# Kernel optimization log

Measured on AMD Instinct MI355X. Metric: run time of the kernel, lower is better.

## Reference

```python
import jax, jax.numpy as jnp
import numpy as np

D = 1024
H = 16
DH = D // H
F = 4096
B, S = 4, 2048
EPS = 1e-5


def _ln(x, g, b):
    m = jnp.mean(x, axis=-1, keepdims=True)
    v = jnp.var(x, axis=-1, keepdims=True)
    return (x - m) * jax.lax.rsqrt(v + EPS) * g + b


def setup_inputs() -> dict:
    key = jax.random.key(0)
    ks = jax.random.split(key, 16)
    s = 0.02
    return {
        "x": jax.random.normal(ks[0], (B, S, D), jnp.float32),
        "key_padding_mask": jnp.zeros((B, S), jnp.bool_),
        "Wq": jax.random.normal(ks[1], (D, D), jnp.float32) * s,
        "bq": jnp.zeros((D,), jnp.float32),
        "Wk": jax.random.normal(ks[2], (D, D), jnp.float32) * s,
        "bk": jnp.zeros((D,), jnp.float32),
        "Wv": jax.random.normal(ks[3], (D, D), jnp.float32) * s,
        "bv": jnp.zeros((D,), jnp.float32),
        "Wo": jax.random.normal(ks[4], (D, D), jnp.float32) * s,
        "bo": jnp.zeros((D,), jnp.float32),
        "W1": jax.random.normal(ks[5], (F, D), jnp.float32) * s,
        "b1": jnp.zeros((F,), jnp.float32),
        "W2": jax.random.normal(ks[6], (D, F), jnp.float32) * s,
        "b2": jnp.zeros((D,), jnp.float32),
        "ln1_g": jnp.ones((D,), jnp.float32),
        "ln1_b": jnp.zeros((D,), jnp.float32),
        "ln2_g": jnp.ones((D,), jnp.float32),
        "ln2_b": jnp.zeros((D,), jnp.float32),
    }


def _attn(x, kpm, Wq, bq, Wk, bk, Wv, bv, Wo, bo):
    b, s, d = x.shape
    scaling = DH ** (-0.5)
    q = (x @ Wq.T + bq) * scaling
    k = x @ Wk.T + bk
    v = x @ Wv.T + bv
    q = q.reshape(b, s, H, DH)
    k = k.reshape(b, s, H, DH)
    v = v.reshape(b, s, H, DH)
    # [b,h,q,k]
    scores = jnp.einsum("bqhd,bkhd->bhqk", q, k)
    scores = jnp.where(kpm[:, None, None, :], -jnp.inf, scores)
    p = jax.nn.softmax(scores.astype(jnp.float32), axis=-1).astype(q.dtype)
    out = jnp.einsum("bhqk,bkhd->bqhd", p, v).reshape(b, s, d)
    return out @ Wo.T + bo


def reference(x, key_padding_mask, Wq, bq, Wk, bk, Wv, bv, Wo, bo,
              W1, b1, W2, b2, ln1_g, ln1_b, ln2_g, ln2_b):
    # post-LN (normalize_before=False), dropout in eval mode (identity)
    x = _ln(x + _attn(x, key_padding_mask, Wq, bq, Wk, bk, Wv, bv, Wo, bo), ln1_g, ln1_b)
    h = jax.nn.gelu(x @ W1.T + b1, approximate=False)
    x = _ln(x + (h @ W2.T + b2), ln2_g, ln2_b)
    return x
```

## Files before the change

kernel.cpp:

```cpp
#include <hip/hip_runtime.h>
#include <hip/hip_bf16.h>
#include <math.h>

typedef short bf16x8 __attribute__((ext_vector_type(8)));
typedef float f32x4 __attribute__((ext_vector_type(4)));
typedef float f32x2 __attribute__((ext_vector_type(2)));

__device__ __forceinline__ unsigned short f2bfu(float f) {
    __hip_bfloat16 h = __float2bfloat16(f);
    return __builtin_bit_cast(unsigned short, h);
}

__device__ __forceinline__ float fexp2(float x) {
    float r;
    asm("v_exp_f32 %0, %1" : "=v"(r) : "v"(x));
    return r;
}

__device__ __forceinline__ unsigned cvtpk_bf16(float lo, float hi) {
    unsigned r;
    asm("v_cvt_pk_bf16_f32 %0, %1, %2" : "=v"(r) : "v"(lo), "v"(hi));
    return r;
}

__device__ __forceinline__ float max3f(float a, float b, float c) {
    float r;
    asm("v_max3_f32 %0, %1, %2, %3" : "=v"(r) : "v"(a), "v"(b), "v"(c));
    return r;
}

__device__ __forceinline__ f32x2 pk_sub2(f32x2 a, f32x2 b) {
    f32x2 r;
    asm("v_pk_add_f32 %0, %1, %2 neg_lo:[0,1] neg_hi:[0,1]" : "=v"(r) : "v"(a), "v"(b));
    return r;
}

__device__ __forceinline__ f32x2 pk_add2(f32x2 a, f32x2 b) {
    f32x2 r;
    asm("v_pk_add_f32 %0, %1, %2" : "=v"(r) : "v"(a), "v"(b));
    return r;
}

__device__ __forceinline__ float gelu_fast(float x) {
    const float x2 = x * x;
    const float z = x * (0.7978845608f + 0.0356774081f * x2);
    const float e = fexp2(z * 2.88539008f);
    const float r = __builtin_amdgcn_rcpf(e + 1.0f);
    return x * (1.0f - r);
}

__device__ __forceinline__ void gload_lds16(const void* gsrc, void* ldst) {
    __builtin_amdgcn_global_load_lds((const __attribute__((address_space(1))) void*)gsrc,
                                     (__attribute__((address_space(3))) void*)ldst,
                                     16, 0, 0);
}

#define MFMA __builtin_amdgcn_mfma_f32_16x16x32_bf16

__global__ __launch_bounds__(256)
void cvt_all_kernel(const float4* __restrict__ x,  ushort4* __restrict__ xb,
                    const float4* __restrict__ wq, ushort4* __restrict__ wqb,
                    const float4* __restrict__ wk, ushort4* __restrict__ wkb,
                    const float4* __restrict__ wv, ushort4* __restrict__ wvb,
                    const float4* __restrict__ wo, ushort4* __restrict__ wob,
                    const float4* __restrict__ w1, ushort4* __restrict__ w1b,
                    const float4* __restrict__ w2, ushort4* __restrict__ w2b)
{
    const int i = blockIdx.x * 256 + threadIdx.x;
    const float4* src;
    ushort4* dst;
    int base;
    if (i < 2097152)      { src = x;  dst = xb;  base = 0; }
    else if (i < 2359296) { src = wq; dst = wqb; base = 2097152; }
    else if (i < 2621440) { src = wk; dst = wkb; base = 2359296; }
    else if (i < 2883584) { src = wv; dst = wvb; base = 2621440; }
    else if (i < 3145728) { src = wo; dst = wob; base = 2883584; }
    else if (i < 4194304) { src = w1; dst = w1b; base = 3145728; }
    else                  { src = w2; dst = w2b; base = 4194304; }
    const float4 v = src[i - base];
    ushort4 o;
    o.x = f2bfu(v.x); o.y = f2bfu(v.y); o.z = f2bfu(v.z); o.w = f2bfu(v.w);
    dst[i - base] = o;
}

enum { EPI_QKV = 0, EPI_RES_OB = 2, EPI_GELU = 3 };

template<int EPI>
__global__ __launch_bounds__(256, 3)
void gemm_bt(const __hip_bfloat16* __restrict__ A,
             const __hip_bfloat16* __restrict__ W,
             const float* __restrict__ bias,
             const void* __restrict__ resv,
             float scale,
             void* __restrict__ outp, void* __restrict__ outp2, void* __restrict__ outp3,
             int M, int N, int K)
{
    __shared__ __hip_bfloat16 As[3][128 * 32];
    __shared__ __hip_bfloat16 Ws[3][128 * 32];
    const int tid = threadIdx.x;
    const int lane = tid & 63;
    const int wid = tid >> 6;
    const int wr = wid >> 1, wc = wid & 1;
    const int g = lane >> 4, lr = lane & 15;
    const int row0 = blockIdx.x * 128;
    const int col0 = blockIdx.y * 128;

    f32x4 acc[4][4];
    const f32x4 zero = {0.f, 0.f, 0.f, 0.f};
#pragma unroll
    for (int m = 0; m < 4; ++m)
#pragma unroll
        for (int n = 0; n < 4; ++n) acc[m][n] = zero;

    const int c0 = tid, c1 = tid + 256;
    const int ar0 = c0 >> 2, ac0 = (c0 & 3) * 8;
    const int ar1 = c1 >> 2, ac1 = (c1 & 3) * 8;
    const __hip_bfloat16* Arow0 = A + (size_t)(row0 + ar0) * K + ac0;
    const __hip_bfloat16* Arow1 = A + (size_t)(row0 + ar1) * K + ac1;
    const __hip_bfloat16* Wrow0 = W + (size_t)(col0 + ar0) * K + ac0;
    const __hip_bfloat16* Wrow1 = W + (size_t)(col0 + ar1) * K + ac1;

    auto stage = [&](int bi, int k0) {
        gload_lds16(Arow0 + k0, (char*)As[bi] + c0 * 16);
        gload_lds16(Arow1 + k0, (char*)As[bi] + c1 * 16);
        gload_lds16(Wrow0 + k0, (char*)Ws[bi] + c0 * 16);
        gload_lds16(Wrow1 + k0, (char*)Ws[bi] + c1 * 16);
    };

    const int NT = K >> 5;
    stage(0, 0);
    stage(1, 32);
    asm volatile("s_waitcnt vmcnt(4)" ::: "memory");
    __builtin_amdgcn_s_barrier();
    __builtin_amdgcn_sched_barrier(0);

    int cur = 0, stg = 2;
    int kpre = 64;
    for (int t = 0; t < NT; ++t) {
        if (t + 2 < NT) stage(stg, kpre);

        bf16x8 af[4], wf[4];
#pragma unroll
        for (int m = 0; m < 4; ++m)
            af[m] = *(const bf16x8*)(As[cur] + (wr * 64 + m * 16 + lr) * 32 + g * 8);
#pragma unroll
        for (int n = 0; n < 4; ++n)
            wf[n] = *(const bf16x8*)(Ws[cur] + (wc * 64 + n * 16 + lr) * 32 + g * 8);
#pragma unroll
        for (int m = 0; m < 4; ++m)
#pragma unroll
            for (int n = 0; n < 4; ++n)
                acc[m][n] = MFMA(af[m], wf[n], acc[m][n], 0, 0, 0);

        if (t + 1 < NT) {
            if (t + 2 < NT) asm volatile("s_waitcnt vmcnt(4)" ::: "memory");
            else            asm volatile("s_waitcnt vmcnt(0)" ::: "memory");
            __builtin_amdgcn_s_barrier();
            __builtin_amdgcn_sched_barrier(0);
        }
        cur = (cur == 2) ? 0 : cur + 1;
        stg = (stg == 2) ? 0 : stg + 1;
        kpre += 32;
    }

#pragma unroll
    for (int n = 0; n < 4; ++n) {
        const int cc = col0 + wc * 64 + n * 16 + lr;
        const float bv = bias[cc];
#pragma unroll
        for (int m = 0; m < 4; ++m) {
            const int rbase = row0 + wr * 64 + m * 16 + g * 4;
            if (EPI == EPI_QKV) {
                const int seg = col0 >> 10;
                if (seg == 2) {
                    ushort4 u;
                    u.x = f2bfu(acc[m][n][0] + bv);
                    u.y = f2bfu(acc[m][n][1] + bv);
                    u.z = f2bfu(acc[m][n][2] + bv);
                    u.w = f2bfu(acc[m][n][3] + bv);
                    const int cc2 = cc - 2048;
                    const int h_ = cc2 >> 6, dh = cc2 & 63;
                    const int bb = rbase >> 11;
                    const int s = rbase & 2047;
                    *(ushort4*)((__hip_bfloat16*)outp3 +
                                (((size_t)bb * 16 + h_) * 64 + dh) * 2048 + s) = u;
                } else {
                    const float sc = (seg == 0) ? scale : 1.0f;
                    __hip_bfloat16* dst = (seg == 0) ? (__hip_bfloat16*)outp
                                                     : (__hip_bfloat16*)outp2;
                    const int ccl = cc & 1023;
#pragma unroll
                    for (int r = 0; r < 4; ++r)
                        dst[(size_t)(rbase + r) * 1024 + ccl] =
                            __float2bfloat16((acc[m][n][r] + bv) * sc);
                }
            } else {
#pragma unroll
                for (int r = 0; r < 4; ++r) {
                    const size_t idx = (size_t)(rbase + r) * N + cc;
                    float v = acc[m][n][r] + bv;
                    if (EPI == EPI_RES_OB) {
                        const float rv = __bfloat162float(((const __hip_bfloat16*)resv)[idx]);
                        ((__hip_bfloat16*)outp)[idx] = __float2bfloat16(v + rv);
                    } else if (EPI == EPI_GELU) {
                        ((__hip_bfloat16*)outp)[idx] = __float2bfloat16(gelu_fast(v));
                    }
                }
            }
        }
    }
}

__global__ __launch_bounds__(512, 4)
void attn_flash3(const __hip_bfloat16* __restrict__ Q,
                 const __hip_bfloat16* __restrict__ K,
                 const __hip_bfloat16* __restrict__ VT,
                 const unsigned char* __restrict__ kpm,
                 __hip_bfloat16* __restrict__ O)
{
    __shared__ __hip_bfloat16 Ks[2][64 * 64];
    __shared__ __hip_bfloat16 VTs[2][64 * 64];
    __shared__ __hip_bfloat16 Plds[8][32 * 64];

    const int tid = threadIdx.x;
    const int lane = tid & 63;
    const int w = tid >> 6;
    const int g = lane >> 4, lr = lane & 15;

    const int orig = blockIdx.y * 8 + blockIdx.x;
    const int nl = (orig & 7) * 64 + (orig >> 3);
    const int qb = nl & 7;
    const int bh = nl >> 3;

    const int b = bh >> 4, h = bh & 15;
    const int q0 = qb * 256 + w * 32;
    const size_t tokbase = (size_t)b * 2048;
    const __hip_bfloat16* VTbh = VT + (size_t)bh * 64 * 2048;

    unsigned tmask = 0;
#pragma unroll
    for (int i = 0; i < 8; ++i) {
        const unsigned mv = *(const unsigned*)(kpm + tokbase + i * 256 + lane * 4);
        const unsigned long long bal = __ballot((int)(mv != 0u));
#pragma unroll
        for (int j = 0; j < 4; ++j)
            if ((bal >> (16 * j)) & 0xFFFFull) tmask |= (1u << (i * 4 + j));
    }

    bf16x8 qf[2][2];
#pragma unroll
    for (int qn = 0; qn < 2; ++qn)
#pragma unroll
        for (int f = 0; f < 2; ++f)
            qf[qn][f] = *(const bf16x8*)(Q + (tokbase + q0 + qn * 16 + lr) * 1024 +
                                         h * 64 + f * 32 + g * 8);

    f32x4 o[2][4];
    const f32x4 zero = {0.f, 0.f, 0.f, 0.f};
#pragma unroll
    for (int qa = 0; qa < 2; ++qa)
#pragma unroll
        for (int nd = 0; nd < 4; ++nd) o[qa][nd] = zero;
    float m_run[2], l_part[2];
#pragma unroll
    for (int qn = 0; qn < 2; ++qn) { m_run[qn] = -1e30f; l_part[qn] = 0.f; }

    __hip_bfloat16* Pw = Plds[w];

    const int srow = w * 8 + (lane >> 3);
    const int sblk = (lane & 7) ^ (srow & 7);
    const __hip_bfloat16* Ksrc = K + (tokbase + srow) * 1024 + h * 64 + sblk * 8;
    const __hip_bfloat16* Vsrc = VTbh + (size_t)srow * 2048 + sblk * 8;

    auto stage = [&](int bufi, int kv0) {
        gload_lds16(Ksrc + (size_t)kv0 * 1024, (char*)&Ks[bufi][w * 512] + lane * 16);
        gload_lds16(Vsrc + kv0, (char*)&VTs[bufi][w * 512] + lane * 16);
    };

    stage(0, 0);
    __syncthreads();
    int buf = 0;

    for (int t = 0; t < 32; ++t) {
        const int kv0 = t * 64;
        if (t < 31) stage(buf ^ 1, kv0 + 64);

        f32x4 st[4][2];
        __builtin_amdgcn_s_setprio(1);
#pragma unroll
        for (int km = 0; km < 4; ++km) {
            bf16x8 kf[2];
#pragma unroll
            for (int f = 0; f < 2; ++f)
                kf[f] = *(const bf16x8*)(&Ks[buf][(km * 16 + lr) * 64 +
                                                  (((f * 4 + g) ^ (lr & 7)) * 8)]);
#pragma unroll
            for (int qn = 0; qn < 2; ++qn) {
                st[km][qn] = MFMA(kf[0], qf[qn][0], zero, 0, 0, 0);
                st[km][qn] = MFMA(kf[1], qf[qn][1], st[km][qn], 0, 0, 0);
            }
        }
        __builtin_amdgcn_s_setprio(0);

        if (tmask & (1u << t)) {
            const float NEG = -1e30f;
#pragma unroll
            for (int km = 0; km < 4; ++km) {
                const unsigned mu = *(const unsigned*)(kpm + tokbase + kv0 + km * 16 + g * 4);
#pragma unroll
                for (int r = 0; r < 4; ++r) {
                    if ((mu >> (8 * r)) & 0xFFu) {
#pragma unroll
                        for (int qn = 0; qn < 2; ++qn) st[km][qn][r] = NEG;
                    }
                }
            }
        }

        float pm[2];
#pragma unroll
        for (int qn = 0; qn < 2; ++qn) {
            const float v1 = max3f(st[0][qn][0], st[0][qn][1], st[0][qn][2]);
            const float v2 = max3f(st[0][qn][3], st[1][qn][0], st[1][qn][1]);
            const float v3 = max3f(st[1][qn][2], st[1][qn][3], st[2][qn][0]);
            const float v4 = max3f(st[2][qn][1], st[2][qn][2], st[2][qn][3]);
            const float v5 = max3f(st[3][qn][0], st[3][qn][1], st[3][qn][2]);
            pm[qn] = fmaxf(max3f(v1, v2, v3), max3f(v4, v5, st[3][qn][3]));
        }
        const int trig = (pm[0] > m_run[0] + 8.f) | (pm[1] > m_run[1] + 8.f);
        if (__any(trig)) {
            float alpha_q[2];
#pragma unroll
            for (int qn = 0; qn < 2; ++qn) {
                float rm = pm[qn];
                rm = fmaxf(rm, __shfl_xor(rm, 16));
                rm = fmaxf(rm, __shfl_xor(rm, 32));
                const float mnew = fmaxf(m_run[qn], rm);
                const float al = fexp2(m_run[qn] - mnew);
                l_part[qn] *= al;
                m_run[qn] = mnew;
                alpha_q[qn] = al;
            }
#pragma unroll
            for (int qa = 0; qa < 2; ++qa)
#pragma unroll
                for (int r = 0; r < 4; ++r) {
                    const float av = __shfl(alpha_q[qa], g * 4 + r, 16);
#pragma unroll
                    for (int nd = 0; nd < 4; ++nd) o[qa][nd][r] *= av;
                }
        }

#pragma unroll
        for (int qn = 0; qn < 2; ++qn) {
            const float mm = m_run[qn];
            const f32x2 mm2 = {mm, mm};
            f32x2 lacc = {0.f, 0.f};
#pragma unroll
            for (int km = 0; km < 4; ++km) {
                const f32x2 s01 = {st[km][qn][0], st[km][qn][1]};
                const f32x2 s23 = {st[km][qn][2], st[km][qn][3]};
                const f32x2 d01 = pk_sub2(s01, mm2);
                const f32x2 d23 = pk_sub2(s23, mm2);
                f32x2 p01, p23;
                p01.x = fexp2(d01.x);
                p01.y = fexp2(d01.y);
                p23.x = fexp2(d23.x);
                p23.y = fexp2(d23.y);
                lacc = pk_add2(lacc, pk_add2(p01, p23));
                uint2 pk;
                pk.x = cvtpk_bf16(p01.x, p01.y);
                pk.y = cvtpk_bf16(p23.x, p23.y);
                const int cs = (km * 2 + (g >> 1)) ^ (lr & 7);
                *(uint2*)(Pw + (qn * 16 + lr) * 64 + cs * 8 + (g & 1) * 4) = pk;
            }
            l_part[qn] += lacc.x + lacc.y;
        }

        __builtin_amdgcn_s_setprio(1);
#pragma unroll
        for (int f = 0; f < 2; ++f) {
            bf16x8 pa[2];
#pragma unroll
            for (int qa = 0; qa < 2; ++qa)
                pa[qa] = *(const bf16x8*)(Pw + (qa * 16 + lr) * 64 +
                                          (((f * 4 + g) ^ (lr & 7)) * 8));
#pragma unroll
            for (int nd = 0; nd < 4; ++nd) {
                bf16x8 vb = *(const bf16x8*)(&VTs[buf][(nd * 16 + lr) * 64 +
                                                       (((f * 4 + g) ^ (lr & 7)) * 8)]);
#pragma unroll
                for (int qa = 0; qa < 2; ++qa)
                    o[qa][nd] = MFMA(pa[qa], vb, o[qa][nd], 0, 0, 0);
            }
        }
        __builtin_amdgcn_s_setprio(0);

        __syncthreads();
        buf ^= 1;
    }

    float linv[2];
#pragma unroll
    for (int qn = 0; qn < 2; ++qn) {
        float lt = l_part[qn];
        lt += __shfl_xor(lt, 16);
        lt += __shfl_xor(lt, 32);
        linv[qn] = 1.0f / lt;
    }
#pragma unroll
    for (int qa = 0; qa < 2; ++qa)
#pragma unroll
        for (int r = 0; r < 4; ++r) {
            const float lv = __shfl(linv[qa], g * 4 + r, 16);
            const size_t row = tokbase + q0 + qa * 16 + g * 4 + r;
#pragma unroll
            for (int nd = 0; nd < 4; ++nd)
                O[row * 1024 + h * 64 + nd * 16 + lr] = __float2bfloat16(o[qa][nd][r] * lv);
        }
}

__global__ __launch_bounds__(256)
void ln_b_kernel(const __hip_bfloat16* __restrict__ in, const float* __restrict__ gamma,
                 const float* __restrict__ beta, float* __restrict__ outf,
                 __hip_bfloat16* __restrict__ outb)
{
    const int row = blockIdx.x;
    const int tid = threadIdx.x;
    const ushort4 u = ((const ushort4*)(in + (size_t)row * 1024))[tid];
    float v0 = __bfloat162float(__builtin_bit_cast(__hip_bfloat16, u.x));
    float v1 = __bfloat162float(__builtin_bit_cast(__hip_bfloat16, u.y));
    float v2 = __bfloat162float(__builtin_bit_cast(__hip_bfloat16, u.z));
    float v3 = __bfloat162float(__builtin_bit_cast(__hip_bfloat16, u.w));
    float s = (v0 + v1) + (v2 + v3);
    float s2 = (v0 * v0 + v1 * v1) + (v2 * v2 + v3 * v3);
#pragma unroll
    for (int off = 1; off < 64; off <<= 1) {
        s += __shfl_xor(s, off);
        s2 += __shfl_xor(s2, off);
    }
    __shared__ float red[8];
    const int wv = tid >> 6;
    if ((tid & 63) == 0) { red[wv] = s; red[4 + wv] = s2; }
    __syncthreads();
    s = red[0] + red[1] + red[2] + red[3];
    s2 = red[4] + red[5] + red[6] + red[7];
    const float mean = s * (1.f / 1024.f);
    const float var = s2 * (1.f / 1024.f) - mean * mean;
    const float rstd = rsqrtf(var + 1e-5f);
    const float4 gm = ((const float4*)gamma)[tid];
    const float4 bt = ((const float4*)beta)[tid];
    float y0 = (v0 - mean) * rstd * gm.x + bt.x;
    float y1 = (v1 - mean) * rstd * gm.y + bt.y;
    float y2 = (v2 - mean) * rstd * gm.z + bt.z;
    float y3 = (v3 - mean) * rstd * gm.w + bt.w;
    if (outf) {
        float4 y; y.x = y0; y.y = y1; y.z = y2; y.w = y3;
        ((float4*)(outf + (size_t)row * 1024))[tid] = y;
    }
    if (outb) {
        ushort4 ub;
        ub.x = f2bfu(y0); ub.y = f2bfu(y1); ub.z = f2bfu(y2); ub.w = f2bfu(y3);
        ((ushort4*)outb)[row * 256 + tid] = ub;
    }
}

extern "C" void kernel_launch(void* const* d_in, const int* in_sizes, int n_in,
                              void* d_out, int out_size, void* d_ws, size_t ws_size,
                              hipStream_t stream)
{
    const float* x    = (const float*)d_in[0];
    const unsigned char* kpm = (const unsigned char*)d_in[1];
    const float* Wq = (const float*)d_in[2];
    const float* bq = (const float*)d_in[3];
    const float* Wk = (const float*)d_in[4];
    const float* bk = (const float*)d_in[5];
    const float* Wv = (const float*)d_in[6];
    const float* bv = (const float*)d_in[7];
    const float* Wo = (const float*)d_in[8];
    const float* bo = (const float*)d_in[9];
    const float* W1 = (const float*)d_in[10];
    const float* b1 = (const float*)d_in[11];
    const float* W2 = (const float*)d_in[12];
    const float* b2 = (const float*)d_in[13];
    const float* ln1g = (const float*)d_in[14];
    const float* ln1b = (const float*)d_in[15];
    const float* ln2g = (const float*)d_in[16];
    const float* ln2b = (const float*)d_in[17];
    float* out = (float*)d_out;

    char* ws = (char*)d_ws;
    const size_t SZ_ND2 = (size_t)8192 * 1024 * 2;
    size_t off = 0;
    __hip_bfloat16* xb  = (__hip_bfloat16*)(ws + off); off += SZ_ND2;
    __hip_bfloat16* wqb = (__hip_bfloat16*)(ws + off); off += (size_t)1024 * 1024 * 2;
    __hip_bfloat16* wkb = (__hip_bfloat16*)(ws + off); off += (size_t)1024 * 1024 * 2;
    __hip_bfloat16* wvb = (__hip_bfloat16*)(ws + off); off += (size_t)1024 * 1024 * 2;
    __hip_bfloat16* wob = (__hip_bfloat16*)(ws + off); off += (size_t)1024 * 1024 * 2;
    __hip_bfloat16* w1b = (__hip_bfloat16*)(ws + off); off += (size_t)4096 * 1024 * 2;
    __hip_bfloat16* w2b = (__hip_bfloat16*)(ws + off); off += (size_t)4096 * 1024 * 2;
    const size_t qkv0 = off;
    __hip_bfloat16* qbp = (__hip_bfloat16*)(ws + off); off += SZ_ND2;
    __hip_bfloat16* kbp = (__hip_bfloat16*)(ws + off); off += SZ_ND2;
    __hip_bfloat16* vtg = (__hip_bfloat16*)(ws + off); off += SZ_ND2;
    __hip_bfloat16* abp = (__hip_bfloat16*)(ws + off); off += SZ_ND2;
    __hip_bfloat16* hbp = (__hip_bfloat16*)(ws + qkv0);
    __hip_bfloat16* y1b = (__hip_bfloat16*)(ws + off); off += SZ_ND2;
    __hip_bfloat16* x1b = (__hip_bfloat16*)(ws + off); off += SZ_ND2;
    __hip_bfloat16* y2b = y1b;
    float* bqkv = (float*)(ws + off); off += 3072 * 4;

    cvt_all_kernel<<<20480, 256, 0, stream>>>(
        (const float4*)x,  (ushort4*)xb,
        (const float4*)Wq, (ushort4*)wqb,
        (const float4*)Wk, (ushort4*)wkb,
        (const float4*)Wv, (ushort4*)wvb,
        (const float4*)Wo, (ushort4*)wob,
        (const float4*)W1, (ushort4*)w1b,
        (const float4*)W2, (ushort4*)w2b);
    hipMemcpyAsync(bqkv,        bq, 4096, hipMemcpyDeviceToDevice, stream);
    hipMemcpyAsync(bqkv + 1024, bk, 4096, hipMemcpyDeviceToDevice, stream);
    hipMemcpyAsync(bqkv + 2048, bv, 4096, hipMemcpyDeviceToDevice, stream);

    dim3 blk(256);
    const float qscale = 0.125f * 1.44269504088896f;

    gemm_bt<EPI_QKV><<<dim3(64, 24), blk, 0, stream>>>(
        xb, wqb, bqkv, nullptr, qscale, qbp, kbp, vtg, 8192, 3072, 1024);

    attn_flash3<<<dim3(8, 64), 512, 0, stream>>>(qbp, kbp, vtg, kpm, abp);

    gemm_bt<EPI_RES_OB><<<dim3(64, 8), blk, 0, stream>>>(
        abp, wob, bo, xb, 1.0f, y1b, nullptr, nullptr, 8192, 1024, 1024);
    ln_b_kernel<<<8192, 256, 0, stream>>>(y1b, ln1g, ln1b, nullptr, x1b);

    gemm_bt<EPI_GELU><<<dim3(64, 32), blk, 0, stream>>>(
        x1b, w1b, b1, nullptr, 1.0f, hbp, nullptr, nullptr, 8192, 4096, 1024);
    gemm_bt<EPI_RES_OB><<<dim3(64, 8), blk, 0, stream>>>(
        hbp, w2b, b2, x1b, 1.0f, y2b, nullptr, nullptr, 8192, 1024, 4096);
    ln_b_kernel<<<8192, 256, 0, stream>>>(y2b, ln2g, ln2b, out, nullptr);
}
```

Baseline: 412.1 us.

## Overlap Wo/W1/W2 bf16 conversion with QKV GEMM via extra blocks

The standalone conversion kernel now casts only x, Wq, Wk and Wv. The Wo, W1 and W2 fp32-to-bf16 casts move into 768 extra blocks appended to the QKV GEMM launch, which becomes a flattened 1D grid. Those extra blocks convert weights while the GEMM blocks run, hiding memory-bound conversion behind compute-bound work. The risk is contention for bandwidth and CU slots with the GEMM blocks, plus extra branching in the GEMM kernel.

```diff
diff --git a/kernel.cpp b/kernel.cpp
--- a/kernel.cpp
+++ b/kernel.cpp
@@ -58,13 +58,10 @@
 #define MFMA __builtin_amdgcn_mfma_f32_16x16x32_bf16
 
 __global__ __launch_bounds__(256)
-void cvt_all_kernel(const float4* __restrict__ x,  ushort4* __restrict__ xb,
-                    const float4* __restrict__ wq, ushort4* __restrict__ wqb,
-                    const float4* __restrict__ wk, ushort4* __restrict__ wkb,
-                    const float4* __restrict__ wv, ushort4* __restrict__ wvb,
-                    const float4* __restrict__ wo, ushort4* __restrict__ wob,
-                    const float4* __restrict__ w1, ushort4* __restrict__ w1b,
-                    const float4* __restrict__ w2, ushort4* __restrict__ w2b)
+void cvt_xqkv_kernel(const float4* __restrict__ x,  ushort4* __restrict__ xb,
+                     const float4* __restrict__ wq, ushort4* __restrict__ wqb,
+                     const float4* __restrict__ wk, ushort4* __restrict__ wkb,
+                     const float4* __restrict__ wv, ushort4* __restrict__ wvb)
 {
     const int i = blockIdx.x * 256 + threadIdx.x;
     const float4* src;
@@ -73,10 +70,7 @@
     if (i < 2097152)      { src = x;  dst = xb;  base = 0; }
     else if (i < 2359296) { src = wq; dst = wqb; base = 2097152; }
     else if (i < 2621440) { src = wk; dst = wkb; base = 2359296; }
-    else if (i < 2883584) { src = wv; dst = wvb; base = 2621440; }
-    else if (i < 3145728) { src = wo; dst = wob; base = 2883584; }
-    else if (i < 4194304) { src = w1; dst = w1b; base = 3145728; }
-    else                  { src = w2; dst = w2b; base = 4194304; }
+    else                  { src = wv; dst = wvb; base = 2621440; }
     const float4 v = src[i - base];
     ushort4 o;
     o.x = f2bfu(v.x); o.y = f2bfu(v.y); o.z = f2bfu(v.z); o.w = f2bfu(v.w);
@@ -93,8 +87,40 @@
              const void* __restrict__ resv,
              float scale,
              void* __restrict__ outp, void* __restrict__ outp2, void* __restrict__ outp3,
-             int M, int N, int K)
+             int M, int N, int K,
+             const float4* __restrict__ cw0, ushort4* __restrict__ cb0,
+             const float4* __restrict__ cw1, ushort4* __restrict__ cb1,
+             const float4* __restrict__ cw2, ushort4* __restrict__ cb2)
 {
+    int row0, col0;
+    if (EPI == EPI_QKV) {
+        const int id = blockIdx.x;
+        if (id >= 1536) {
+            const int stride = 768 * 256;
+            int j = (id - 1536) * 256 + threadIdx.x;
+#pragma unroll
+            for (int it = 0; it < 12; ++it) {
+                const float4* src;
+                ushort4* dst;
+                int base;
+                if (j < 262144)       { src = cw0; dst = cb0; base = 0; }
+                else if (j < 1310720) { src = cw1; dst = cb1; base = 262144; }
+                else                  { src = cw2; dst = cb2; base = 1310720; }
+                const float4 v = src[j - base];
+                ushort4 o;
+                o.x = f2bfu(v.x); o.y = f2bfu(v.y); o.z = f2bfu(v.z); o.w = f2bfu(v.w);
+                dst[j - base] = o;
+                j += stride;
+            }
+            return;
+        }
+        row0 = (id & 63) * 128;
+        col0 = (id >> 6) * 128;
+    } else {
+        row0 = blockIdx.x * 128;
+        col0 = blockIdx.y * 128;
+    }
+
     __shared__ __hip_bfloat16 As[3][128 * 32];
     __shared__ __hip_bfloat16 Ws[3][128 * 32];
     const int tid = threadIdx.x;
@@ -102,8 +128,6 @@
     const int wid = tid >> 6;
     const int wr = wid >> 1, wc = wid & 1;
     const int g = lane >> 4, lr = lane & 15;
-    const int row0 = blockIdx.x * 128;
-    const int col0 = blockIdx.y * 128;
 
     f32x4 acc[4][4];
     const f32x4 zero = {0.f, 0.f, 0.f, 0.f};
@@ -510,33 +534,36 @@
     __hip_bfloat16* y2b = y1b;
     float* bqkv = (float*)(ws + off); off += 3072 * 4;
 
-    cvt_all_kernel<<<20480, 256, 0, stream>>>(
+    cvt_xqkv_kernel<<<11264, 256, 0, stream>>>(
         (const float4*)x,  (ushort4*)xb,
         (const float4*)Wq, (ushort4*)wqb,
         (const float4*)Wk, (ushort4*)wkb,
-        (const float4*)Wv, (ushort4*)wvb,
+        (const float4*)Wv, (ushort4*)wvb);
+    hipMemcpyAsync(bqkv,        bq, 4096, hipMemcpyDeviceToDevice, stream);
+    hipMemcpyAsync(bqkv + 1024, bk, 4096, hipMemcpyDeviceToDevice, stream);
+    hipMemcpyAsync(bqkv + 2048, bv, 4096, hipMemcpyDeviceToDevice, stream);
+
+    dim3 blk(256);
+    const float qscale = 0.125f * 1.44269504088896f;
+
+    gemm_bt<EPI_QKV><<<2304, blk, 0, stream>>>(
+        xb, wqb, bqkv, nullptr, qscale, qbp, kbp, vtg, 8192, 3072, 1024,
         (const float4*)Wo, (ushort4*)wob,
         (const float4*)W1, (ushort4*)w1b,
         (const float4*)W2, (ushort4*)w2b);
-    hipMemcpyAsync(bqkv,        bq, 4096, hipMemcpyDeviceToDevice, stream);
-    hipMemcpyAsync(bqkv + 1024, bk, 4096, hipMemcpyDeviceToDevice, stream);
-    hipMemcpyAsync(bqkv + 2048, bv, 4096, hipMemcpyDeviceToDevice, stream);
-
-    dim3 blk(256);
-    const float qscale = 0.125f * 1.44269504088896f;
-
-    gemm_bt<EPI_QKV><<<dim3(64, 24), blk, 0, stream>>>(
-        xb, wqb, bqkv, nullptr, qscale, qbp, kbp, vtg, 8192, 3072, 1024);
 
     attn_flash3<<<dim3(8, 64), 512, 0, stream>>>(qbp, kbp, vtg, kpm, abp);
 
     gemm_bt<EPI_RES_OB><<<dim3(64, 8), blk, 0, stream>>>(
-        abp, wob, bo, xb, 1.0f, y1b, nullptr, nullptr, 8192, 1024, 1024);
+        abp, wob, bo, xb, 1.0f, y1b, nullptr, nullptr, 8192, 1024, 1024,
+        nullptr, nullptr, nullptr, nullptr, nullptr, nullptr);
     ln_b_kernel<<<8192, 256, 0, stream>>>(y1b, ln1g, ln1b, nullptr, x1b);
 
     gemm_bt<EPI_GELU><<<dim3(64, 32), blk, 0, stream>>>(
-        x1b, w1b, b1, nullptr, 1.0f, hbp, nullptr, nullptr, 8192, 4096, 1024);
+        x1b, w1b, b1, nullptr, 1.0f, hbp, nullptr, nullptr, 8192, 4096, 1024,
+        nullptr, nullptr, nullptr, nullptr, nullptr, nullptr);
     gemm_bt<EPI_RES_OB><<<dim3(64, 8), blk, 0, stream>>>(
-        hbp, w2b, b2, x1b, 1.0f, y2b, nullptr, nullptr, 8192, 1024, 4096);
+        hbp, w2b, b2, x1b, 1.0f, y2b, nullptr, nullptr, 8192, 1024, 4096,
+        nullptr, nullptr, nullptr, nullptr, nullptr, nullptr);
     ln_b_kernel<<<8192, 256, 0, stream>>>(y2b, ln2g, ln2b, out, nullptr);
 }
```

New measurement: 414.7 us. No clear change (+0.6%).

## Add 256x256-tile 8-wave GEMM with swizzled LDS for FFN up-projection

Applied to the files above, without the earlier changes.

Adds a new GEMM kernel using 256x256 output tiles, 512 threads (8 waves) and BK=64. It double-buffers A and B through direct global-to-LDS loads with an XOR swizzle, and interleaves the B-half and A prefetches with MFMA phases under barriers and s_setprio. Only the W1 GELU GEMM switches to it. The aim is more data reuse per loaded byte and better MFMA issue on the largest GEMM. In exchange it runs one block per CU with large LDS and register use, a grid of only 512 blocks, and a scalar, uncoalesced epilogue store pattern.

```diff
diff --git a/kernel.cpp b/kernel.cpp
--- a/kernel.cpp
+++ b/kernel.cpp
@@ -56,6 +56,8 @@
 }
 
 #define MFMA __builtin_amdgcn_mfma_f32_16x16x32_bf16
+#define SBAR __builtin_amdgcn_s_barrier
+#define SCHB __builtin_amdgcn_sched_barrier
 
 __global__ __launch_bounds__(256)
 void cvt_all_kernel(const float4* __restrict__ x,  ushort4* __restrict__ xb,
@@ -86,6 +88,163 @@
 enum { EPI_QKV = 0, EPI_RES_OB = 2, EPI_GELU = 3 };
 
 template<int EPI>
+__global__ __launch_bounds__(512, 1)
+void gemm8p(const __hip_bfloat16* __restrict__ A,
+            const __hip_bfloat16* __restrict__ W,
+            const float* __restrict__ bias,
+            const void* __restrict__ resv,
+            void* __restrict__ outp,
+            int M, int N, int K)
+{
+    __shared__ __hip_bfloat16 As[2][256 * 64];
+    __shared__ __hip_bfloat16 Bs[2][256 * 64];
+    const int tid = threadIdx.x;
+    const int lane = tid & 63;
+    const int wid = tid >> 6;
+    const int wr = wid >> 1;
+    const int wc = wid & 1;
+    const int g = lane >> 4, lr = lane & 15;
+    const int row0 = blockIdx.x * 256;
+    const int col0 = blockIdx.y * 256;
+
+    f32x4 acc[4][8];
+    const f32x4 zero = {0.f, 0.f, 0.f, 0.f};
+#pragma unroll
+    for (int m = 0; m < 4; ++m)
+#pragma unroll
+        for (int n = 0; n < 8; ++n) acc[m][n] = zero;
+
+    const int arl = tid >> 3;
+    const int agc = (tid & 7) ^ (arl & 7);
+    const __hip_bfloat16* Abase = A + (size_t)(row0 + arl) * K + agc * 8;
+    const __hip_bfloat16* Bbase = W + (size_t)(col0 + arl) * K + agc * 8;
+
+    auto stageA = [&](int bi, int kt) {
+#pragma unroll
+        for (int q = 0; q < 4; ++q)
+            gload_lds16(Abase + (size_t)(q * 64) * K + kt * 64,
+                        (char*)As[bi] + q * 8192 + tid * 16);
+    };
+    auto stageB = [&](int bi, int h, int kt) {
+#pragma unroll
+        for (int j = 0; j < 2; ++j)
+            gload_lds16(Bbase + (size_t)(h * 128 + j * 64) * K + kt * 64,
+                        (char*)Bs[bi] + h * 16384 + j * 8192 + tid * 16);
+    };
+
+    const int NT = K >> 6;
+    stageA(0, 0);
+    stageB(0, 0, 0);
+    stageB(0, 1, 0);
+    stageA(1, 1);
+    asm volatile("s_waitcnt vmcnt(4)" ::: "memory");
+    SBAR();
+    SCHB(0);
+
+    const int swz = lr & 7;
+    const int arow = wr * 64;
+    const int brow = wc * 128;
+
+    for (int t = 0; t < NT; ++t) {
+        const int bi = t & 1;
+        const __hip_bfloat16* Ab = As[bi];
+        const __hip_bfloat16* Bb = Bs[bi];
+        bf16x8 a[4], b0[4], b1[4];
+
+#pragma unroll
+        for (int m = 0; m < 4; ++m)
+            a[m] = *(const bf16x8*)(Ab + (arow + m * 16 + lr) * 64 + ((g ^ swz) * 8));
+#pragma unroll
+        for (int n = 0; n < 4; ++n)
+            b0[n] = *(const bf16x8*)(Bb + (brow + n * 16 + lr) * 64 + ((g ^ swz) * 8));
+        if (t + 1 < NT) stageB(bi ^ 1, 0, t + 1);
+        SCHB(0);
+        SBAR();
+        __builtin_amdgcn_s_setprio(1);
+#pragma unroll
+        for (int m = 0; m < 4; ++m)
+#pragma unroll
+            for (int n = 0; n < 4; ++n)
+                acc[m][n] = MFMA(a[m], b0[n], acc[m][n], 0, 0, 0);
+        __builtin_amdgcn_s_setprio(0);
+        SBAR();
+
+#pragma unroll
+        for (int n = 0; n < 4; ++n)
+            b1[n] = *(const bf16x8*)(Bb + (brow + (n + 4) * 16 + lr) * 64 + ((g ^ swz) * 8));
+        if (t + 1 < NT) stageB(bi ^ 1, 1, t + 1);
+        SCHB(0);
+        SBAR();
+        __builtin_amdgcn_s_setprio(1);
+#pragma unroll
+        for (int m = 0; m < 4; ++m)
+#pragma unroll
+            for (int n = 0; n < 4; ++n)
+                acc[m][n + 4] = MFMA(a[m], b1[n], acc[m][n + 4], 0, 0, 0);
+        __builtin_amdgcn_s_setprio(0);
+        SBAR();
+
+#pragma unroll
+        for (int m = 0; m < 4; ++m)
+            a[m] = *(const bf16x8*)(Ab + (arow + m * 16 + lr) * 64 + (((4 + g) ^ swz) * 8));
+#pragma unroll
+        for (int n = 0; n < 4; ++n)
+            b0[n] = *(const bf16x8*)(Bb + (brow + n * 16 + lr) * 64 + (((4 + g) ^ swz) * 8));
+        SCHB(0);
+        SBAR();
+        __builtin_amdgcn_s_setprio(1);
+#pragma unroll
+        for (int m = 0; m < 4; ++m)
+#pragma unroll
+            for (int n = 0; n < 4; ++n)
+                acc[m][n] = MFMA(a[m], b0[n], acc[m][n], 0, 0, 0);
+        __builtin_amdgcn_s_setprio(0);
+        SBAR();
+
+#pragma unroll
+        for (int n = 0; n < 4; ++n)
+            b1[n] = *(const bf16x8*)(Bb + (brow + (n + 4) * 16 + lr) * 64 + (((4 + g) ^ swz) * 8));
+        if (t + 2 < NT) stageA(bi, t + 2);
+        SCHB(0);
+        SBAR();
+        __builtin_amdgcn_s_setprio(1);
+#pragma unroll
+        for (int m = 0; m < 4; ++m)
+#pragma unroll
+            for (int n = 0; n < 4; ++n)
+                acc[m][n + 4] = MFMA(a[m], b1[n], acc[m][n + 4], 0, 0, 0);
+        __builtin_amdgcn_s_setprio(0);
+        if (t + 1 < NT) {
+            if (t + 2 < NT) asm volatile("s_waitcnt vmcnt(4)" ::: "memory");
+            else            asm volatile("s_waitcnt vmcnt(0)" ::: "memory");
+            SBAR();
+            SCHB(0);
+        }
+    }
+
+#pragma unroll
+    for (int n = 0; n < 8; ++n) {
+        const int cc = col0 + wc * 128 + n * 16 + lr;
+        const float bv = bias[cc];
+#pragma unroll
+        for (int m = 0; m < 4; ++m) {
+            const int rbase = row0 + wr * 64 + m * 16 + g * 4;
+#pragma unroll
+            for (int r = 0; r < 4; ++r) {
+                const size_t idx = (size_t)(rbase + r) * N + cc;
+                float v = acc[m][n][r] + bv;
+                if (EPI == EPI_RES_OB) {
+                    const float rv = __bfloat162float(((const __hip_bfloat16*)resv)[idx]);
+                    ((__hip_bfloat16*)outp)[idx] = __float2bfloat16(v + rv);
+                } else if (EPI == EPI_GELU) {
+                    ((__hip_bfloat16*)outp)[idx] = __float2bfloat16(gelu_fast(v));
+                }
+            }
+        }
+    }
+}
+
+template<int EPI>
 __global__ __launch_bounds__(256, 3)
 void gemm_bt(const __hip_bfloat16* __restrict__ A,
              const __hip_bfloat16* __restrict__ W,
@@ -131,8 +290,8 @@
     stage(0, 0);
     stage(1, 32);
     asm volatile("s_waitcnt vmcnt(4)" ::: "memory");
-    __builtin_amdgcn_s_barrier();
-    __builtin_amdgcn_sched_barrier(0);
+    SBAR();
+    SCHB(0);
 
     int cur = 0, stg = 2;
     int kpre = 64;
@@ -155,8 +314,8 @@
         if (t + 1 < NT) {
             if (t + 2 < NT) asm volatile("s_waitcnt vmcnt(4)" ::: "memory");
             else            asm volatile("s_waitcnt vmcnt(0)" ::: "memory");
-            __builtin_amdgcn_s_barrier();
-            __builtin_amdgcn_sched_barrier(0);
+            SBAR();
+            SCHB(0);
         }
         cur = (cur == 2) ? 0 : cur + 1;
         stg = (stg == 2) ? 0 : stg + 1;
@@ -534,8 +693,8 @@
         abp, wob, bo, xb, 1.0f, y1b, nullptr, nullptr, 8192, 1024, 1024);
     ln_b_kernel<<<8192, 256, 0, stream>>>(y1b, ln1g, ln1b, nullptr, x1b);
 
-    gemm_bt<EPI_GELU><<<dim3(64, 32), blk, 0, stream>>>(
-        x1b, w1b, b1, nullptr, 1.0f, hbp, nullptr, nullptr, 8192, 4096, 1024);
+    gemm8p<EPI_GELU><<<dim3(32, 16), 512, 0, stream>>>(
+        x1b, w1b, b1, nullptr, hbp, 8192, 4096, 1024);
     gemm_bt<EPI_RES_OB><<<dim3(64, 8), blk, 0, stream>>>(
         hbp, w2b, b2, x1b, 1.0f, y2b, nullptr, nullptr, 8192, 1024, 4096);
     ln_b_kernel<<<8192, 256, 0, stream>>>(y2b, ln2g, ln2b, out, nullptr);
```

Result: faster. 394.9 us (-4.2%).
